# Optimization experiments

Hardware: AMD Instinct MI355X
Metric: run time of the kernel (lower is better)

The kernel has to match this reference:

```python
import jax, jax.numpy as jnp
import numpy as np

LUT_N = 16 * 17 * 17 * 17  # 78608, covers max index 16*(16*17*17 + 16*17 + 16) = 78592
H = W = 2048


def setup_inputs() -> dict:
    key = jax.random.key(0)
    k1, k2, k3, k4 = jax.random.split(key, 4)
    # quantized pixel values in [0, 16], stored as float like the torch module expects
    x_in = jax.random.randint(k1, (1, 3, H, W), 0, 17).astype(jnp.float32)
    x_s = jax.random.randint(k2, (1, 3, H, W), 0, 17).astype(jnp.float32)
    # int8 LUT tables of shape [N, 20, 1, 1]
    feature_msb = jax.random.randint(k3, (LUT_N, 20, 1, 1), -32, 32).astype(jnp.int8)
    feature_lsb = jax.random.randint(k4, (LUT_N, 20, 1, 1), -32, 32).astype(jnp.int8)
    return {"x_in": x_in, "x_s": x_s, "feature_msb": feature_msb, "feature_lsb": feature_lsb}


def reference(x_in, x_s, feature_msb, feature_lsb):
    B, C, Hh, Ww = x_in.shape
    # index weights: [16*17*17, 16*17, 16], broadcast over (1,3,1,1)
    weights = jnp.array([16 * 17 * 17, 16 * 17, 16], dtype=jnp.float32).reshape(1, 3, 1, 1)
    idx_msb = jnp.sum(x_in * weights, axis=1).reshape(-1).astype(jnp.int32)  # [B*H*W]
    idx_lsb = jnp.sum(x_s * weights, axis=1).reshape(-1).astype(jnp.int32)
    nfeat = feature_msb.shape[1]  # 20
    # gather -> (1, H, W, 20) -> (1, 20, H, W), cast to float as in torch .float()
    out_msb = feature_msb[idx_msb].reshape(1, Hh, Ww, nfeat).transpose(0, 3, 1, 2).astype(jnp.float32)
    out_lsb = feature_lsb[idx_lsb].reshape(1, Hh, Ww, nfeat).transpose(0, 3, 1, 2).astype(jnp.float32)
    out = out_msb + out_lsb
    # AdaptiveAvgPool2d(1) == global mean over H, W
    out = jnp.mean(out, axis=(2, 3), keepdims=True)  # (1, 20, 1, 1)
    # quantize to 0.25 steps and clamp to [-32, 31.75]
    out = jnp.clip(jnp.round(out * 4.0) / 4.0, -32.0, 31.75)
    return out
```

## Files before the change

kernel.cpp:

```cpp
#include <hip/hip_runtime.h>


#define NBINS 4913
#define NPIX  (2048 * 2048)
#define G4    (NPIX / 4)
#define NFEAT 20
#define MAIN_BLOCKS 1024

__global__ __launch_bounds__(256) void compact_k(const int* __restrict__ msb,
                                                 const int* __restrict__ lsb,
                                                 int* __restrict__ cm,
                                                 int* __restrict__ cl) {
    int ok = 1;
    for (int i = 0; i < 64; ++i) {
        int v = msb[i];
        ok &= (v >= -32 && v < 32);
    }
    const bool is_int32 = (ok != 0);

    const int total = NBINS * 5;
    int t = blockIdx.x * 256 + threadIdx.x;
    const int stride = gridDim.x * 256;
    for (; t < total; t += stride) {
        int j = t / 5;
        int k = t - j * 5;
        int wm, wl;
        if (is_int32) {
            const int* rm = msb + j * 320 + k * 4;
            const int* rl = lsb + j * 320 + k * 4;
            unsigned um = (unsigned)(rm[0] & 0xff) | ((unsigned)(rm[1] & 0xff) << 8) |
                          ((unsigned)(rm[2] & 0xff) << 16) | ((unsigned)(rm[3] & 0xff) << 24);
            unsigned ul = (unsigned)(rl[0] & 0xff) | ((unsigned)(rl[1] & 0xff) << 8) |
                          ((unsigned)(rl[2] & 0xff) << 16) | ((unsigned)(rl[3] & 0xff) << 24);
            wm = (int)um;
            wl = (int)ul;
        } else {
            wm = msb[j * 80 + k];
            wl = lsb[j * 80 + k];
        }
        cm[t] = wm;
        cl[t] = wl;
    }
}

__global__ __launch_bounds__(256) void feat_main(const float* __restrict__ xin,
                                                 const float* __restrict__ xs,
                                                 const int* __restrict__ cm,
                                                 const int* __restrict__ cl,
                                                 int* __restrict__ partial) {
    __shared__ int hist[2 * NBINS];
    __shared__ int wsum[4][NFEAT];
    for (int i = threadIdx.x; i < 2 * NBINS; i += 256) hist[i] = 0;
    __syncthreads();

    const float4* a = (const float4*)xin;
    const float4* b = (const float4*)xs;
    const int nt = MAIN_BLOCKS * 256;
    for (int g = blockIdx.x * 256 + threadIdx.x; g < G4; g += nt) {
        float4 a0 = a[g], a1 = a[g + G4], a2 = a[g + 2 * G4];
        float4 b0 = b[g], b1 = b[g + G4], b2 = b[g + 2 * G4];

        int m0 = (int)fmaf(a0.x, 289.0f, fmaf(a1.x, 17.0f, a2.x));
        int m1 = (int)fmaf(a0.y, 289.0f, fmaf(a1.y, 17.0f, a2.y));
        int m2 = (int)fmaf(a0.z, 289.0f, fmaf(a1.z, 17.0f, a2.z));
        int m3 = (int)fmaf(a0.w, 289.0f, fmaf(a1.w, 17.0f, a2.w));
        int s0 = (int)fmaf(b0.x, 289.0f, fmaf(b1.x, 17.0f, b2.x));
        int s1 = (int)fmaf(b0.y, 289.0f, fmaf(b1.y, 17.0f, b2.y));
        int s2 = (int)fmaf(b0.z, 289.0f, fmaf(b1.z, 17.0f, b2.z));
        int s3 = (int)fmaf(b0.w, 289.0f, fmaf(b1.w, 17.0f, b2.w));

        atomicAdd(&hist[m0], 1);
        atomicAdd(&hist[m1], 1);
        atomicAdd(&hist[m2], 1);
        atomicAdd(&hist[m3], 1);
        atomicAdd(&hist[NBINS + s0], 1);
        atomicAdd(&hist[NBINS + s1], 1);
        atomicAdd(&hist[NBINS + s2], 1);
        atomicAdd(&hist[NBINS + s3], 1);
    }
    __syncthreads();

    int acc[NFEAT];
#pragma unroll
    for (int f = 0; f < NFEAT; ++f) acc[f] = 0;

    for (int j = threadIdx.x; j < NBINS; j += 256) {
        int hm = hist[j];
        int hl = hist[NBINS + j];
        if (hm) {
            const int* r = cm + j * 5;
#pragma unroll
            for (int k = 0; k < 5; ++k) {
                int w = r[k];
                acc[4 * k + 0] += hm * ((w << 24) >> 24);
                acc[4 * k + 1] += hm * ((w << 16) >> 24);
                acc[4 * k + 2] += hm * ((w << 8) >> 24);
                acc[4 * k + 3] += hm * (w >> 24);
            }
        }
        if (hl) {
            const int* r = cl + j * 5;
#pragma unroll
            for (int k = 0; k < 5; ++k) {
                int w = r[k];
                acc[4 * k + 0] += hl * ((w << 24) >> 24);
                acc[4 * k + 1] += hl * ((w << 16) >> 24);
                acc[4 * k + 2] += hl * ((w << 8) >> 24);
                acc[4 * k + 3] += hl * (w >> 24);
            }
        }
    }

    const int lane = threadIdx.x & 63;
    const int wv = threadIdx.x >> 6;
#pragma unroll
    for (int f = 0; f < NFEAT; ++f) {
        int v = acc[f];
#pragma unroll
        for (int o = 32; o > 0; o >>= 1) v += __shfl_xor(v, o, 64);
        if (lane == 0) wsum[wv][f] = v;
    }
    __syncthreads();
    if (threadIdx.x < NFEAT) {
        int f = threadIdx.x;
        partial[blockIdx.x * NFEAT + f] = wsum[0][f] + wsum[1][f] + wsum[2][f] + wsum[3][f];
    }
}

__global__ __launch_bounds__(64) void finalize_k(const int* __restrict__ partial,
                                                 float* __restrict__ out) {
    const int f = blockIdx.x;
    const int lane = threadIdx.x;
    int s = 0;
    for (int b = lane; b < MAIN_BLOCKS; b += 64) s += partial[b * NFEAT + f];
#pragma unroll
    for (int o = 32; o > 0; o >>= 1) s += __shfl_xor(s, o, 64);
    if (lane == 0) {
        double m4 = (double)s * (1.0 / 1048576.0);
        double r = rint(m4);
        float v = (float)(r * 0.25);
        v = fminf(fmaxf(v, -32.0f), 31.75f);
        out[f] = v;
    }
}

extern "C" void kernel_launch(void* const* d_in, const int* in_sizes, int n_in,
                              void* d_out, int out_size, void* d_ws, size_t ws_size,
                              hipStream_t stream) {
    const float* xin = (const float*)d_in[0];
    const float* xs = (const float*)d_in[1];
    const int* msb = (const int*)d_in[2];
    const int* lsb = (const int*)d_in[3];
    float* out = (float*)d_out;

    int* cm = (int*)d_ws;
    int* cl = (int*)((char*)d_ws + 98304);
    int* partial = (int*)((char*)d_ws + 2 * 98304);

    compact_k<<<96, 256, 0, stream>>>(msb, lsb, cm, cl);
    feat_main<<<MAIN_BLOCKS, 256, 0, stream>>>(xin, xs, cm, cl, partial);
    finalize_k<<<NFEAT, 64, 0, stream>>>(partial, out);
}
```

Before: 157.3 us.

## Pack dual histograms into one LDS array and fuse finalize via last-block reduction

The msb and lsb histograms now share a single shared-memory array, each bin holding two 16-bit counts (lsb counts added as 1<<16), which halves LDS use. The compacted LUT is interleaved into 12-int rows so each bin's weights load as three int4 reads. Blocks grow to 512 threads with a fixed two-iteration loop. The separate finalize kernel is replaced by an atomic counter, so the last block reduces all partials and writes the output, saving a launch. The 16-bit packing relies on each block seeing few enough pixels that no bin count overflows, and the counter reset inside compact_k relies on launch order on the stream.

```diff
diff --git a/kernel.cpp b/kernel.cpp
--- a/kernel.cpp
+++ b/kernel.cpp
@@ -5,12 +5,16 @@
 #define NPIX  (2048 * 2048)
 #define G4    (NPIX / 4)
 #define NFEAT 20
-#define MAIN_BLOCKS 1024
+#define MB    1024
+#define MT    512
+
 
 __global__ __launch_bounds__(256) void compact_k(const int* __restrict__ msb,
                                                  const int* __restrict__ lsb,
-                                                 int* __restrict__ cm,
-                                                 int* __restrict__ cl) {
+                                                 int* __restrict__ cc,
+                                                 unsigned* __restrict__ counter) {
+    if (blockIdx.x == 0 && threadIdx.x == 0) *counter = 0u;
+
     int ok = 1;
     for (int i = 0; i < 64; ++i) {
         int v = msb[i];
@@ -18,45 +22,55 @@
     }
     const bool is_int32 = (ok != 0);
 
-    const int total = NBINS * 5;
+    const int total = NBINS * 10;
     int t = blockIdx.x * 256 + threadIdx.x;
-    const int stride = gridDim.x * 256;
-    for (; t < total; t += stride) {
-        int j = t / 5;
-        int k = t - j * 5;
-        int wm, wl;
-        if (is_int32) {
-            const int* rm = msb + j * 320 + k * 4;
-            const int* rl = lsb + j * 320 + k * 4;
-            unsigned um = (unsigned)(rm[0] & 0xff) | ((unsigned)(rm[1] & 0xff) << 8) |
-                          ((unsigned)(rm[2] & 0xff) << 16) | ((unsigned)(rm[3] & 0xff) << 24);
-            unsigned ul = (unsigned)(rl[0] & 0xff) | ((unsigned)(rl[1] & 0xff) << 8) |
-                          ((unsigned)(rl[2] & 0xff) << 16) | ((unsigned)(rl[3] & 0xff) << 24);
-            wm = (int)um;
-            wl = (int)ul;
-        } else {
-            wm = msb[j * 80 + k];
-            wl = lsb[j * 80 + k];
-        }
-        cm[t] = wm;
-        cl[t] = wl;
+    if (t >= total) return;
+    int j = t / 10;
+    int k = t - j * 10;
+    const int* base = (k < 5) ? msb : lsb;
+    int kk = (k < 5) ? k : k - 5;
+    int w;
+    if (is_int32) {
+        const int* r = base + j * 320 + kk * 4;
+        w = (int)((unsigned)(r[0] & 0xff) | ((unsigned)(r[1] & 0xff) << 8) |
+                  ((unsigned)(r[2] & 0xff) << 16) | ((unsigned)(r[3] & 0xff) << 24));
+    } else {
+        w = base[j * 80 + kk];
     }
+    cc[j * 12 + k] = w;
 }
 
-__global__ __launch_bounds__(256) void feat_main(const float* __restrict__ xin,
-                                                 const float* __restrict__ xs,
-                                                 const int* __restrict__ cm,
-                                                 const int* __restrict__ cl,
-                                                 int* __restrict__ partial) {
-    __shared__ int hist[2 * NBINS];
-    __shared__ int wsum[4][NFEAT];
-    for (int i = threadIdx.x; i < 2 * NBINS; i += 256) hist[i] = 0;
+#define SX(w, sh) ((int)((unsigned)(w) << (sh)) >> 24)
+#define MACW(h, w, base)                                \
+    acc[(base) + 0] += __mul24((h), SX((w), 24));       \
+    acc[(base) + 1] += __mul24((h), SX((w), 16));       \
+    acc[(base) + 2] += __mul24((h), SX((w), 8));        \
+    acc[(base) + 3] += __mul24((h), ((int)(w) >> 24));
+
+__device__ __forceinline__ int wave_red(int v) {
+#pragma unroll
+    for (int o = 32; o > 0; o >>= 1) v += __shfl_xor(v, o, 64);
+    return v;
+}
+
+__global__ __launch_bounds__(MT, 8) void feat_main(const float* __restrict__ xin,
+                                                   const float* __restrict__ xs,
+                                                   const int* __restrict__ cc,
+                                                   int* __restrict__ partial,
+                                                   unsigned* __restrict__ counter,
+                                                   float* __restrict__ out) {
+    __shared__ int hist[NBINS];
+    __shared__ int wsum[MT / 64][NFEAT];
+    __shared__ unsigned last_s;
+
+    for (int i = threadIdx.x; i < NBINS; i += MT) hist[i] = 0;
     __syncthreads();
 
     const float4* a = (const float4*)xin;
     const float4* b = (const float4*)xs;
-    const int nt = MAIN_BLOCKS * 256;
-    for (int g = blockIdx.x * 256 + threadIdx.x; g < G4; g += nt) {
+    int g = blockIdx.x * MT + threadIdx.x;
+#pragma unroll
+    for (int it = 0; it < 2; ++it) {
         float4 a0 = a[g], a1 = a[g + G4], a2 = a[g + 2 * G4];
         float4 b0 = b[g], b1 = b[g + G4], b2 = b[g + 2 * G4];
 
@@ -73,10 +87,11 @@
         atomicAdd(&hist[m1], 1);
         atomicAdd(&hist[m2], 1);
         atomicAdd(&hist[m3], 1);
-        atomicAdd(&hist[NBINS + s0], 1);
-        atomicAdd(&hist[NBINS + s1], 1);
-        atomicAdd(&hist[NBINS + s2], 1);
-        atomicAdd(&hist[NBINS + s3], 1);
+        atomicAdd(&hist[s0], 1 << 16);
+        atomicAdd(&hist[s1], 1 << 16);
+        atomicAdd(&hist[s2], 1 << 16);
+        atomicAdd(&hist[s3], 1 << 16);
+        g += MB * MT;
     }
     __syncthreads();
 
@@ -84,63 +99,61 @@
 #pragma unroll
     for (int f = 0; f < NFEAT; ++f) acc[f] = 0;
 
-    for (int j = threadIdx.x; j < NBINS; j += 256) {
-        int hm = hist[j];
-        int hl = hist[NBINS + j];
-        if (hm) {
-            const int* r = cm + j * 5;
-#pragma unroll
-            for (int k = 0; k < 5; ++k) {
-                int w = r[k];
-                acc[4 * k + 0] += hm * ((w << 24) >> 24);
-                acc[4 * k + 1] += hm * ((w << 16) >> 24);
-                acc[4 * k + 2] += hm * ((w << 8) >> 24);
-                acc[4 * k + 3] += hm * (w >> 24);
-            }
-        }
-        if (hl) {
-            const int* r = cl + j * 5;
-#pragma unroll
-            for (int k = 0; k < 5; ++k) {
-                int w = r[k];
-                acc[4 * k + 0] += hl * ((w << 24) >> 24);
-                acc[4 * k + 1] += hl * ((w << 16) >> 24);
-                acc[4 * k + 2] += hl * ((w << 8) >> 24);
-                acc[4 * k + 3] += hl * (w >> 24);
-            }
-        }
+    for (int j = threadIdx.x; j < NBINS; j += MT) {
+        int h = hist[j];
+        int hm = h & 0xffff;
+        int hl = (int)((unsigned)h >> 16);
+        const int4* r = (const int4*)(cc + j * 12);
+        int4 q0 = r[0], q1 = r[1], q2 = r[2];
+        MACW(hm, q0.x, 0)  MACW(hm, q0.y, 4)  MACW(hm, q0.z, 8)
+        MACW(hm, q0.w, 12) MACW(hm, q1.x, 16)
+        MACW(hl, q1.y, 0)  MACW(hl, q1.z, 4)  MACW(hl, q1.w, 8)
+        MACW(hl, q2.x, 12) MACW(hl, q2.y, 16)
     }
 
     const int lane = threadIdx.x & 63;
     const int wv = threadIdx.x >> 6;
 #pragma unroll
     for (int f = 0; f < NFEAT; ++f) {
-        int v = acc[f];
-#pragma unroll
-        for (int o = 32; o > 0; o >>= 1) v += __shfl_xor(v, o, 64);
+        int v = wave_red(acc[f]);
         if (lane == 0) wsum[wv][f] = v;
     }
     __syncthreads();
     if (threadIdx.x < NFEAT) {
-        int f = threadIdx.x;
-        partial[blockIdx.x * NFEAT + f] = wsum[0][f] + wsum[1][f] + wsum[2][f] + wsum[3][f];
+        int s = 0;
+#pragma unroll
+        for (int w = 0; w < MT / 64; ++w) s += wsum[w][threadIdx.x];
+        partial[blockIdx.x * NFEAT + threadIdx.x] = s;
     }
-}
 
-__global__ __launch_bounds__(64) void finalize_k(const int* __restrict__ partial,
-                                                 float* __restrict__ out) {
-    const int f = blockIdx.x;
-    const int lane = threadIdx.x;
-    int s = 0;
-    for (int b = lane; b < MAIN_BLOCKS; b += 64) s += partial[b * NFEAT + f];
+    __threadfence();
+    __syncthreads();
+    if (threadIdx.x == 0) last_s = atomicAdd(counter, 1u);
+    __syncthreads();
+    if (last_s != MB - 1) return;
+
+    __threadfence();
+    int accf[NFEAT];
+    const int* p0 = partial + threadIdx.x * NFEAT;
+    const int* p1 = partial + (threadIdx.x + MT) * NFEAT;
 #pragma unroll
-    for (int o = 32; o > 0; o >>= 1) s += __shfl_xor(s, o, 64);
-    if (lane == 0) {
+    for (int f = 0; f < NFEAT; ++f) accf[f] = p0[f] + p1[f];
+
+#pragma unroll
+    for (int f = 0; f < NFEAT; ++f) {
+        int v = wave_red(accf[f]);
+        if (lane == 0) wsum[wv][f] = v;
+    }
+    __syncthreads();
+    if (threadIdx.x < NFEAT) {
+        int s = 0;
+#pragma unroll
+        for (int w = 0; w < MT / 64; ++w) s += wsum[w][threadIdx.x];
         double m4 = (double)s * (1.0 / 1048576.0);
         double r = rint(m4);
         float v = (float)(r * 0.25);
         v = fminf(fmaxf(v, -32.0f), 31.75f);
-        out[f] = v;
+        out[threadIdx.x] = v;
     }
 }
 
@@ -153,11 +166,10 @@
     const int* lsb = (const int*)d_in[3];
     float* out = (float*)d_out;
 
-    int* cm = (int*)d_ws;
-    int* cl = (int*)((char*)d_ws + 98304);
-    int* partial = (int*)((char*)d_ws + 2 * 98304);
+    int* cc = (int*)d_ws;
+    int* partial = (int*)((char*)d_ws + 245760);
+    unsigned* counter = (unsigned*)((char*)d_ws + 327680);
 
-    compact_k<<<96, 256, 0, stream>>>(msb, lsb, cm, cl);
-    feat_main<<<MAIN_BLOCKS, 256, 0, stream>>>(xin, xs, cm, cl, partial);
-    finalize_k<<<NFEAT, 64, 0, stream>>>(partial, out);
+    compact_k<<<192, 256, 0, stream>>>(msb, lsb, cc, counter);
+    feat_main<<<MB, MT, 0, stream>>>(xin, xs, cc, partial, counter, out);
 }
```

After: 268.4 us. 70.7% more time.
